# Optimization experiments

Measured on AMD Instinct MI355X. Metric: run time of the kernel, lower is better.

## Reference

```python
import jax, jax.numpy as jnp
import numpy as np

B, T, N, D = 8, 64, 196, 768
K, P = 8, 2
BOUND = 2.5
EPS = 1e-6


def _dct2_basis(T, P, dtype=jnp.float32):
    t = jnp.arange(T, dtype=dtype) + 0.5
    rows = [jnp.ones(T, dtype=dtype)]
    for p in range(1, P + 1):
        rows.append(jnp.cos(jnp.pi * p * t / T))
    Bm = jnp.stack(rows, axis=0)  # [P+1, T]
    return Bm / (jnp.sqrt(jnp.sum(Bm * Bm, axis=1, keepdims=True)) + EPS)


def setup_inputs() -> dict:
    key = jax.random.key(0)
    k1, k2, k3 = jax.random.split(key, 3)
    x = jax.random.normal(k1, (B, T, N, D), dtype=jnp.float32)
    valid_mask = jnp.ones((B, T, N), dtype=jnp.float32)
    # proj weight [K, D]; module orthonormalizes (QR of W.T) every forward,
    # so we materialize the already-orthonormalized parameter value here.
    W0 = jax.random.uniform(k2, (K, D), dtype=jnp.float32, minval=-0.05, maxval=0.05)
    Q, _ = jnp.linalg.qr(W0.T)          # [D, K] orthonormal cols
    proj_W = Q.T                         # [K, D]
    feat_in = K * (P + 3)                # K*(P+1+2) = 40
    bound = float(np.sqrt(6.0 / (feat_in + D)))
    W_raw = jax.random.uniform(k3, (feat_in, D), dtype=jnp.float32, minval=-bound, maxval=bound)
    beta = jnp.full((D,), 0.5, dtype=jnp.float32)
    return {"x": x, "valid_mask": valid_mask, "proj_W": proj_W, "W_raw": W_raw, "beta": beta}


def reference(x, valid_mask, proj_W, W_raw, beta):
    b, t, n, d = x.shape
    U = proj_W.T                                         # [D, K]
    v = jnp.einsum('btnd,dk->btnk', x, U)
    v = v * valid_mask[..., None]
    v_bnkt = jnp.transpose(v, (0, 2, 3, 1))              # [B, N, K, T]
    rms = jnp.sqrt(jnp.mean(v_bnkt * v_bnkt, axis=-1, keepdims=True) + EPS)
    v_bounded = BOUND * jnp.tanh(v_bnkt / (rms + EPS))
    Bmat = _dct2_basis(t, P, x.dtype)                    # [P+1, T]
    coeff = jnp.einsum('bnkt,pt->bnkp', v_bounded, Bmat)
    mean_feat = jnp.mean(v_bounded, axis=-1, keepdims=True)
    rms_feat = jnp.sqrt(jnp.mean(v_bounded * v_bounded, axis=-1, keepdims=True) + EPS)
    feats = jnp.concatenate([coeff, mean_feat, rms_feat], axis=-1).reshape(b, n, -1)  # [B,N,K*(P+3)]
    W = jax.nn.softplus(W_raw)                           # [feat_in, D]
    y = feats @ W                                        # [B, N, D]
    beta_s = jax.nn.sigmoid(beta)[None, None, None, :]
    h = x + beta_s * y[:, None, :, :]
    m = valid_mask[..., None]
    h = m * h + (1.0 - m) * x
    return (h, W)
```

## Files before the change

kernel.cpp:

```cpp
#include <hip/hip_runtime.h>
#include <math.h>

#define B_ 8
#define T_ 64
#define N_ 196
#define D_ 768
#define K_ 8
#define FEAT 40
#define EPSF 1e-6f

constexpr int BN = B_ * N_;
constexpr int ROWS = B_ * T_ * N_;
constexpr long long HSIZE = (long long)ROWS * D_;
constexpr int QPR = D_ / 4;
constexpr unsigned RSTRIDE = (unsigned)N_ * QPR;

typedef float v4f __attribute__((ext_vector_type(4)));

__device__ __forceinline__ float wredux(float v) {
#pragma unroll
    for (int off = 32; off > 0; off >>= 1)
        v += __shfl_xor(v, off, 64);
    return v;
}

__device__ __forceinline__ float dot4(v4f a, v4f b) {
    return a.x * b.x + a.y * b.y + a.z * b.z + a.w * b.w;
}

__global__ __launch_bounds__(256) void k_wsp(const float* __restrict__ wraw,
                                             const float* __restrict__ beta,
                                             float* __restrict__ wout,
                                             float* __restrict__ beta_s) {
    int i = blockIdx.x * blockDim.x + threadIdx.x;
    if (i < FEAT * D_) {
        float xw = wraw[i];
        wout[i] = fmaxf(xw, 0.0f) + log1pf(expf(-fabsf(xw)));
    }
    if (i < D_) beta_s[i] = 1.0f / (1.0f + expf(-beta[i]));
}

__global__ __launch_bounds__(256)
void k_fused(const float* __restrict__ x,
             const float* __restrict__ mask,
             const float* __restrict__ pw,
             const float* __restrict__ wsp,
             const float* __restrict__ beta_s,
             float* __restrict__ h) {
    __shared__ v4f   xbuf[4][QPR];
    __shared__ float vpart[T_][K_ + 1];
    __shared__ float sf[FEAT];
    __shared__ float ylds[D_];
    __shared__ float smask[T_];

    const int tid  = threadIdx.x;
    const int lane = tid & 63;
    const int w    = tid >> 6;
    const int bn   = blockIdx.x;
    const int b    = bn / N_;
    const int n    = bn - b * N_;

    v4f u[2][3];
#pragma unroll
    for (int kk = 0; kk < 2; kk++)
#pragma unroll
        for (int c = 0; c < 3; c++)
            u[kk][c] = *(const v4f*)(pw + (2 * w + kk) * D_ + c * 256 + lane * 4);

    if (tid < T_) smask[tid] = mask[(b * T_ + tid) * N_ + n];

    const v4f* x4 = (const v4f*)x;
    const unsigned TSTRIDE = 4 * RSTRIDE;
    unsigned q = (unsigned)((b * T_ + w) * N_ + n) * QPR;
    v4f R0 = x4[q + lane], R1 = x4[q + 64 + lane], R2 = x4[q + 128 + lane];
#pragma unroll 1
    for (int tile = 0; tile < 16; ++tile) {
        __syncthreads();
        xbuf[w][lane]       = R0;
        xbuf[w][64 + lane]  = R1;
        xbuf[w][128 + lane] = R2;
        if (tile < 15) {
            q += TSTRIDE;
            R0 = x4[q + lane];
            R1 = x4[q + 64 + lane];
            R2 = x4[q + 128 + lane];
        }
        __syncthreads();
#pragma unroll
        for (int r = 0; r < 4; ++r) {
            v4f c0 = xbuf[r][lane];
            v4f c1 = xbuf[r][64 + lane];
            v4f c2 = xbuf[r][128 + lane];
            float a0 = dot4(c0, u[0][0]) + dot4(c1, u[0][1]) + dot4(c2, u[0][2]);
            float a1 = dot4(c0, u[1][0]) + dot4(c1, u[1][1]) + dot4(c2, u[1][2]);
            a0 += __shfl_xor(a0, 1, 64);
            a1 += __shfl_xor(a1, 1, 64);
            float val = (lane & 1) ? a1 : a0;
            val += __shfl_xor(val, 2, 64);
            val += __shfl_xor(val, 4, 64);
            val += __shfl_xor(val, 8, 64);
            val += __shfl_xor(val, 16, 64);
            val += __shfl_xor(val, 32, 64);
            if (lane < 2) vpart[tile * 4 + r][2 * w + lane] = val;
        }
    }
    __syncthreads();

#pragma unroll
    for (int kk = 0; kk < 2; kk++) {
        const int k = w + kk * 4;
        float v = vpart[lane][k] * smask[lane];
        float s2  = wredux(v * v);
        float rms = sqrtf(s2 * (1.0f / T_) + EPSF);
        float vb  = 2.5f * tanhf(v / (rms + EPSF));
        const float PI = 3.14159265358979323846f;
        float ph = PI * ((float)lane + 0.5f) / (float)T_;
        float c1 = cosf(ph), c2 = cosf(2.0f * ph);
        float n1 = wredux(c1 * c1), n2 = wredux(c2 * c2);
        float S1 = wredux(vb), Sc1 = wredux(vb * c1);
        float Sc2 = wredux(vb * c2), Sq = wredux(vb * vb);
        if (lane == 0) {
            float* o = sf + k * 5;
            o[0] = S1 / (8.0f + EPSF);
            o[1] = Sc1 / (sqrtf(n1) + EPSF);
            o[2] = Sc2 / (sqrtf(n2) + EPSF);
            o[3] = S1 * (1.0f / T_);
            o[4] = sqrtf(Sq * (1.0f / T_) + EPSF);
        }
    }
    __syncthreads();

    for (int d = tid; d < D_; d += 256) {
        float a0 = 0.f, a1 = 0.f;
#pragma unroll
        for (int f = 0; f < FEAT; f += 2) {
            a0 += sf[f]     * wsp[f * D_ + d];
            a1 += sf[f + 1] * wsp[(f + 1) * D_ + d];
        }
        ylds[d] = (a0 + a1) * beta_s[d];
    }
    __syncthreads();

    const v4f* y4 = (const v4f*)ylds;
    const v4f y0 = y4[lane], y1 = y4[64 + lane], y2 = y4[128 + lane];
    v4f* h4 = (v4f*)h;
    unsigned qD = (unsigned)((b * T_ + w * 16) * N_ + n) * QPR;
    v4f d0 = __builtin_nontemporal_load(x4 + qD + lane);
    v4f d1 = __builtin_nontemporal_load(x4 + qD + 64 + lane);
    v4f d2 = __builtin_nontemporal_load(x4 + qD + 128 + lane);
#pragma unroll 1
    for (int j = 0; j < 16; j++) {
        v4f c0 = d0, c1 = d1, c2 = d2;
        const unsigned qc = qD;
        if (j < 15) {
            qD += RSTRIDE;
            d0 = __builtin_nontemporal_load(x4 + qD + lane);
            d1 = __builtin_nontemporal_load(x4 + qD + 64 + lane);
            d2 = __builtin_nontemporal_load(x4 + qD + 128 + lane);
        }
        const float m = smask[w * 16 + j];
        __builtin_nontemporal_store(c0 + m * y0, h4 + qc + lane);
        __builtin_nontemporal_store(c1 + m * y1, h4 + qc + 64 + lane);
        __builtin_nontemporal_store(c2 + m * y2, h4 + qc + 128 + lane);
    }
}

extern "C" void kernel_launch(void* const* d_in, const int* in_sizes, int n_in,
                              void* d_out, int out_size, void* d_ws, size_t ws_size,
                              hipStream_t stream) {
    const float* x    = (const float*)d_in[0];
    const float* mask = (const float*)d_in[1];
    const float* pw   = (const float*)d_in[2];
    const float* wraw = (const float*)d_in[3];
    const float* beta = (const float*)d_in[4];

    float* h    = (float*)d_out;
    float* wout = h + HSIZE;
    float* beta_s = (float*)d_ws;

    hipLaunchKernelGGL(k_wsp, dim3((FEAT * D_ + 255) / 256), dim3(256), 0, stream,
                       wraw, beta, wout, beta_s);
    hipLaunchKernelGGL(k_fused, dim3(BN), dim3(256), 0, stream,
                       x, mask, pw, wout, beta_s, h);
}
```

Before: 150.8 us.

## Split fused kernel into projection kernel and separate grid-stride residual update

Splits the single fused kernel into two. k_proj computes the per-(b,n) feature vector y and writes it to workspace. k_final is a new grid-stride streaming kernel that computes h = x + mask*y over all elements. The aim is better memory-level parallelism and full-device occupancy for the write pass, which in the fused version was handled by only 1568 blocks. The cost is a second full read of x, since it is no longer reused while possibly cache-resident, plus an extra launch and 64-bit index division per element.

```diff
diff --git a/kernel.cpp b/kernel.cpp
--- a/kernel.cpp
+++ b/kernel.cpp
@@ -14,6 +14,7 @@
 constexpr long long HSIZE = (long long)ROWS * D_;
 constexpr int QPR = D_ / 4;
 constexpr unsigned RSTRIDE = (unsigned)N_ * QPR;
+constexpr long long QTOT = (long long)ROWS * QPR;
 
 typedef float v4f __attribute__((ext_vector_type(4)));
 
@@ -41,16 +42,15 @@
 }
 
 __global__ __launch_bounds__(256)
-void k_fused(const float* __restrict__ x,
-             const float* __restrict__ mask,
-             const float* __restrict__ pw,
-             const float* __restrict__ wsp,
-             const float* __restrict__ beta_s,
-             float* __restrict__ h) {
+void k_proj(const float* __restrict__ x,
+            const float* __restrict__ mask,
+            const float* __restrict__ pw,
+            const float* __restrict__ wsp,
+            const float* __restrict__ beta_s,
+            float* __restrict__ y_ws) {
     __shared__ v4f   xbuf[4][QPR];
     __shared__ float vpart[T_][K_ + 1];
     __shared__ float sf[FEAT];
-    __shared__ float ylds[D_];
     __shared__ float smask[T_];
 
     const int tid  = threadIdx.x;
@@ -130,38 +130,42 @@
     }
     __syncthreads();
 
-    for (int d = tid; d < D_; d += 256) {
+    float* yrow = y_ws + (size_t)bn * D_;
+#pragma unroll
+    for (int i = 0; i < 3; ++i) {
+        const int d = tid + 256 * i;
         float a0 = 0.f, a1 = 0.f;
 #pragma unroll
         for (int f = 0; f < FEAT; f += 2) {
             a0 += sf[f]     * wsp[f * D_ + d];
             a1 += sf[f + 1] * wsp[(f + 1) * D_ + d];
         }
-        ylds[d] = (a0 + a1) * beta_s[d];
+        yrow[d] = (a0 + a1) * beta_s[d];
     }
-    __syncthreads();
+}
 
-    const v4f* y4 = (const v4f*)ylds;
-    const v4f y0 = y4[lane], y1 = y4[64 + lane], y2 = y4[128 + lane];
+__global__ __launch_bounds__(256)
+void k_final(const float* __restrict__ x,
+             const float* __restrict__ maskv,
+             const float* __restrict__ y_ws,
+             float* __restrict__ h,
+             long long stride) {
+    const v4f* x4 = (const v4f*)x;
+    const v4f* y4 = (const v4f*)y_ws;
     v4f* h4 = (v4f*)h;
-    unsigned qD = (unsigned)((b * T_ + w * 16) * N_ + n) * QPR;
-    v4f d0 = __builtin_nontemporal_load(x4 + qD + lane);
-    v4f d1 = __builtin_nontemporal_load(x4 + qD + 64 + lane);
-    v4f d2 = __builtin_nontemporal_load(x4 + qD + 128 + lane);
-#pragma unroll 1
-    for (int j = 0; j < 16; j++) {
-        v4f c0 = d0, c1 = d1, c2 = d2;
-        const unsigned qc = qD;
-        if (j < 15) {
-            qD += RSTRIDE;
-            d0 = __builtin_nontemporal_load(x4 + qD + lane);
-            d1 = __builtin_nontemporal_load(x4 + qD + 64 + lane);
-            d2 = __builtin_nontemporal_load(x4 + qD + 128 + lane);
-        }
-        const float m = smask[w * 16 + j];
-        __builtin_nontemporal_store(c0 + m * y0, h4 + qc + lane);
-        __builtin_nontemporal_store(c1 + m * y1, h4 + qc + 64 + lane);
-        __builtin_nontemporal_store(c2 + m * y2, h4 + qc + 128 + lane);
+
+    for (long long qq = (long long)blockIdx.x * blockDim.x + threadIdx.x;
+         qq < QTOT; qq += stride) {
+        const int row = (int)(qq / QPR);
+        const int d4  = (int)(qq - (long long)row * QPR);
+        const int b   = row / (T_ * N_);
+        const int rem = row - b * (T_ * N_);
+        const int n   = rem % N_;
+
+        v4f xv = __builtin_nontemporal_load(x4 + qq);
+        float m = maskv[row];
+        v4f yv = y4[(size_t)(b * N_ + n) * QPR + d4];
+        __builtin_nontemporal_store(xv + m * yv, h4 + qq);
     }
 }
 
@@ -176,10 +180,15 @@
 
     float* h    = (float*)d_out;
     float* wout = h + HSIZE;
+
     float* beta_s = (float*)d_ws;
+    float* y_ws   = (float*)d_ws + 1024;
 
     hipLaunchKernelGGL(k_wsp, dim3((FEAT * D_ + 255) / 256), dim3(256), 0, stream,
                        wraw, beta, wout, beta_s);
-    hipLaunchKernelGGL(k_fused, dim3(BN), dim3(256), 0, stream,
-                       x, mask, pw, wout, beta_s, h);
+    hipLaunchKernelGGL(k_proj, dim3(BN), dim3(256), 0, stream,
+                       x, mask, pw, wout, beta_s, y_ws);
+    const int fblocks = 4096;
+    hipLaunchKernelGGL(k_final, dim3(fblocks), dim3(256), 0, stream,
+                       x, mask, y_ws, h, (long long)fblocks * 256);
 }
```

Result: slower. 205.3 us (+36.1%).
